# Kernel optimization log

Measured on AMD Instinct MI355X. Metric: run time of the kernel, lower is better.

The kernel has to match this reference:

```python
import jax, jax.numpy as jnp
import numpy as np

EPS = 1e-6
BLK = 64          # VSA coarse block size
H = 12            # num attention heads


def _ln(x, w=None, b=None):
    m = jnp.mean(x, -1, keepdims=True)
    v = jnp.mean((x - m) ** 2, -1, keepdims=True)
    y = (x - m) * jax.lax.rsqrt(v + EPS)
    return y * w + b if w is not None else y


def _rms(x, w):
    return x * jax.lax.rsqrt(jnp.mean(x * x, -1, keepdims=True) + EPS) * w


def _rope(x, cos, sin):
    # non-neox (interleaved) rotary; x: [B,S,H,D], cos/sin: [S,D/2]
    x1, x2 = x[..., 0::2], x[..., 1::2]
    c, s = cos[None, :, None, :], sin[None, :, None, :]
    return jnp.stack([x1 * c - x2 * s, x2 * c + x1 * s], -1).reshape(x.shape)


def _attn(q, k, v):
    scale = 1.0 / np.sqrt(q.shape[-1])
    p = jax.nn.softmax(jnp.einsum('bshd,bthd->bhst', q, k) * scale, -1)
    return jnp.einsum('bhst,bthd->bshd', p, v)


def setup_inputs() -> dict:
    key = jax.random.key(0)
    ks = jax.random.split(key, 24)
    B, S, L2, DIM, FFN = 1, 2048, 512, 1536, 8960
    D = DIM // H
    # rope tables
    pos = jnp.arange(S, dtype=jnp.float32)
    inv = 1.0 / (10000.0 ** (jnp.arange(D // 2, dtype=jnp.float32) / (D // 2)))
    ang = pos[:, None] * inv[None, :]
    w = lambda k, shape, fan: jax.random.normal(k, shape, jnp.float32) / np.sqrt(fan)
    return {
        'hidden_states': jax.random.normal(ks[0], (B, S, DIM), jnp.float32),
        'encoder_hidden_states': jax.random.normal(ks[1], (B, L2, DIM), jnp.float32),
        'temb': jax.random.normal(ks[2], (B, 6, DIM), jnp.float32),
        'rope_cos': jnp.cos(ang), 'rope_sin': jnp.sin(ang),
        'scale_shift_table': w(ks[3], (1, 6, DIM), DIM),
        'Wq': w(ks[4], (DIM, DIM), DIM), 'bq': jnp.zeros((DIM,), jnp.float32),
        'Wk': w(ks[5], (DIM, DIM), DIM), 'bk': jnp.zeros((DIM,), jnp.float32),
        'Wv': w(ks[6], (DIM, DIM), DIM), 'bv': jnp.zeros((DIM,), jnp.float32),
        'Wg': w(ks[7], (DIM, DIM), DIM), 'bg': jnp.zeros((DIM,), jnp.float32),
        'Wo': w(ks[8], (DIM, DIM), DIM), 'bo': jnp.zeros((DIM,), jnp.float32),
        'nq_w': jnp.ones((DIM,), jnp.float32), 'nk_w': jnp.ones((DIM,), jnp.float32),
        'saln_w': jnp.ones((DIM,), jnp.float32), 'saln_b': jnp.zeros((DIM,), jnp.float32),
        'cWq': w(ks[9], (DIM, DIM), DIM), 'cbq': jnp.zeros((DIM,), jnp.float32),
        'cWk': w(ks[10], (DIM, DIM), DIM), 'cbk': jnp.zeros((DIM,), jnp.float32),
        'cWv': w(ks[11], (DIM, DIM), DIM), 'cbv': jnp.zeros((DIM,), jnp.float32),
        'cWo': w(ks[12], (DIM, DIM), DIM), 'cbo': jnp.zeros((DIM,), jnp.float32),
        'cnq_w': jnp.ones((DIM,), jnp.float32), 'cnk_w': jnp.ones((DIM,), jnp.float32),
        'W1': w(ks[13], (DIM, FFN), DIM), 'b1': jnp.zeros((FFN,), jnp.float32),
        'W2': w(ks[14], (FFN, DIM), FFN), 'b2': jnp.zeros((DIM,), jnp.float32),
    }


def reference(hidden_states, encoder_hidden_states, temb, rope_cos, rope_sin,
              scale_shift_table, Wq, bq, Wk, bk, Wv, bv, Wg, bg, Wo, bo,
              nq_w, nk_w, saln_w, saln_b,
              cWq, cbq, cWk, cbk, cWv, cbv, cWo, cbo, cnq_w, cnk_w,
              W1, b1, W2, b2):
    B, S, DIM = hidden_states.shape
    D = DIM // H
    # AdaLN modulation
    e = scale_shift_table + temb  # [B,6,DIM]
    shift, scale, gate, c_shift, c_scale, c_gate = [e[:, i:i + 1] for i in range(6)]
    x = hidden_states
    n = _ln(x) * (1.0 + scale) + shift
    # QKV + gate_compress projections, RMSNorm across heads on q/k
    q = _rms(n @ Wq + bq, nq_w).reshape(B, S, H, D)
    k = _rms(n @ Wk + bk, nk_w).reshape(B, S, H, D)
    v = (n @ Wv + bv).reshape(B, S, H, D)
    g = (n @ Wg + bg).reshape(B, S, H, D)
    q = _rope(q, rope_cos, rope_sin)
    k = _rope(k, rope_cos, rope_sin)
    # VSA: fine (dense, all blocks selected) + gated coarse (block-mean-pooled)
    fine = _attn(q, k, v)
    Nb = S // BLK
    qc = q.reshape(B, Nb, BLK, H, D).mean(2)
    kc = k.reshape(B, Nb, BLK, H, D).mean(2)
    vc = v.reshape(B, Nb, BLK, H, D).mean(2)
    coarse = jnp.repeat(_attn(qc, kc, vc), BLK, axis=1)  # [B,S,H,D]
    ao = (fine + coarse * g).reshape(B, S, DIM) @ Wo + bo
    # self-attn residual + affine LN (null shift/scale)
    hidden = x + gate * ao
    n2 = _ln(hidden, saln_w, saln_b)
    # T2V cross attention
    cq = _rms(n2 @ cWq + cbq, cnq_w).reshape(B, S, H, D)
    ck = _rms(encoder_hidden_states @ cWk + cbk, cnk_w).reshape(B, -1, H, D)
    cv = (encoder_hidden_states @ cWv + cbv).reshape(B, -1, H, D)
    co = _attn(cq, ck, cv).reshape(B, S, DIM) @ cWo + cbo
    hidden = hidden + co
    n3 = _ln(hidden) * (1.0 + c_scale) + c_shift
    # FFN with tanh-approx GELU, gated residual
    ffn = jax.nn.gelu(n3 @ W1 + b1, approximate=True) @ W2 + b2
    return hidden + c_gate * ffn
```

## Files before the change

### kernel.cpp

```cpp
#include <hip/hip_runtime.h>

#define DIMH 1536
#define NH 12
#define DH 128
#define SQ 2048
#define SKV 512
#define FFNH 8960

typedef short short8v __attribute__((ext_vector_type(8)));
typedef short short4v __attribute__((ext_vector_type(4)));
typedef float f32x4 __attribute__((ext_vector_type(4)));

union U8 { unsigned short u[8]; short8v v; };
union U4 { unsigned short u[4]; short4v v; };

__device__ __forceinline__ unsigned short f2bf(float f) {
  unsigned int u = __float_as_uint(f);
  u += 0x7fffu + ((u >> 16) & 1u);
  return (unsigned short)(u >> 16);
}
__device__ __forceinline__ float bf2f(unsigned short u) {
  return __uint_as_float((unsigned int)u << 16);
}

__device__ __forceinline__ void gld16(const void* g, void* l) {
  __builtin_amdgcn_global_load_lds(
      (const __attribute__((address_space(1))) unsigned int*)g,
      (__attribute__((address_space(3))) unsigned int*)l, 16, 0, 0);
}


__global__ void prep_e(const float* __restrict__ sst, const float* __restrict__ temb,
                       float* __restrict__ e) {
  int i = blockIdx.x * 256 + threadIdx.x;
  if (i < 6 * DIMH) e[i] = sst[i] + temb[i];
}

__global__ void concat4(const float* __restrict__ a, const float* __restrict__ b,
                        const float* __restrict__ c, const float* __restrict__ d,
                        float* __restrict__ o) {
  int i = blockIdx.x * 256 + threadIdx.x;
  int which = i / DIMH, r = i - which * DIMH;
  float v;
  if (which == 0) v = a[r];
  else if (which == 1) v = b[r];
  else if (which == 2) v = c[r];
  else v = d[r];
  o[i] = v;
}

__global__ void cast_f32_bf16(const float* __restrict__ x, unsigned short* __restrict__ y,
                              int n) {
  int i = blockIdx.x * 256 + threadIdx.x;
  if (i < n) y[i] = f2bf(x[i]);
}

__global__ __launch_bounds__(256) void transpose_bf16(const float* __restrict__ W,
    unsigned short* __restrict__ Wt, int K, int N) {
  __shared__ float T[32][33];
  int n0 = blockIdx.x * 32, k0 = blockIdx.y * 32;
  int tx = threadIdx.x & 31, ty = threadIdx.x >> 5;
#pragma unroll
  for (int p = 0; p < 4; p++)
    T[ty + p * 8][tx] = W[(long)(k0 + ty + p * 8) * N + n0 + tx];
  __syncthreads();
#pragma unroll
  for (int p = 0; p < 4; p++)
    Wt[(long)(n0 + ty + p * 8) * K + k0 + tx] = f2bf(T[tx][ty + p * 8]);
}

__global__ __launch_bounds__(256) void vtrans(const unsigned short* __restrict__ v, int vs,
    unsigned short* __restrict__ vt, int S) {
  __shared__ unsigned short T[32][33];
  int s0 = blockIdx.x * 32, c0 = blockIdx.y * 32;
  int tx = threadIdx.x & 31, ty = threadIdx.x >> 5;
#pragma unroll
  for (int p = 0; p < 4; p++)
    T[ty + p * 8][tx] = v[(long)(s0 + ty + p * 8) * vs + c0 + tx];
  __syncthreads();
  int head = c0 / DH, dbase = c0 - head * DH;
#pragma unroll
  for (int p = 0; p < 4; p++)
    vt[(long)head * DH * S + (long)(dbase + ty + p * 8) * S + s0 + tx] = T[tx][ty + p * 8];
}

__device__ __forceinline__ float blockReduceSum(float val) {
  __shared__ float sm[4];
#pragma unroll
  for (int off = 32; off > 0; off >>= 1) val += __shfl_xor(val, off, 64);
  if ((threadIdx.x & 63) == 0) sm[threadIdx.x >> 6] = val;
  __syncthreads();
  val = sm[0] + sm[1] + sm[2] + sm[3];
  __syncthreads();
  return val;
}

__global__ __launch_bounds__(256) void layernorm_affine(const float* __restrict__ x,
    unsigned short* __restrict__ out, const float* __restrict__ g,
    const float* __restrict__ b, float add1) {
  long row = blockIdx.x;
  int tid = threadIdx.x;
  const float* xr = x + row * DIMH;
  float v[6];
  float s = 0.f;
#pragma unroll
  for (int i = 0; i < 6; i++) { v[i] = xr[tid + i * 256]; s += v[i]; }
  s = blockReduceSum(s);
  float mean = s * (1.f / DIMH);
  float s2 = 0.f;
#pragma unroll
  for (int i = 0; i < 6; i++) { float d = v[i] - mean; s2 += d * d; }
  s2 = blockReduceSum(s2);
  float inv = rsqrtf(s2 * (1.f / DIMH) + 1e-6f);
  unsigned short* o = out + row * DIMH;
#pragma unroll
  for (int i = 0; i < 6; i++) {
    int c = tid + i * 256;
    o[c] = f2bf((v[i] - mean) * inv * (g[c] + add1) + b[c]);
  }
}

__global__ __launch_bounds__(256) void rms_rope(unsigned short* __restrict__ x, int xs,
    const float* __restrict__ w, const float* __restrict__ cosb,
    const float* __restrict__ sinb, int do_rope, float sc) {
  __shared__ float xr[DIMH];
  long row = blockIdx.x;
  int tid = threadIdx.x;
  unsigned short* xp = x + row * xs;
  float ss = 0.f;
#pragma unroll
  for (int i = 0; i < 6; i++) {
    float t = bf2f(xp[tid + i * 256]);
    xr[tid + i * 256] = t;
    ss += t * t;
  }
  ss = blockReduceSum(ss);
  float inv = rsqrtf(ss * (1.f / DIMH) + 1e-6f) * sc;
#pragma unroll
  for (int j = 0; j < 3; j++) {
    int p = tid + j * 256;
    int h = p >> 6, i = p & 63;
    int d1 = h * DH + 2 * i;
    float v1 = xr[d1] * inv * w[d1];
    float v2 = xr[d1 + 1] * inv * w[d1 + 1];
    float o1 = v1, o2 = v2;
    if (do_rope) {
      float c = cosb[row * 64 + i], s = sinb[row * 64 + i];
      o1 = v1 * c - v2 * s;
      o2 = v2 * c + v1 * s;
    }
    xp[d1] = f2bf(o1);
    xp[d1 + 1] = f2bf(o2);
  }
}

__global__ void pool64(const unsigned short* __restrict__ src, int ss,
                       float* __restrict__ dst) {
  int c = blockIdx.x * 256 + threadIdx.x;
  int nb = blockIdx.y;
  float s = 0.f;
  for (int j = 0; j < 64; j++) s += bf2f(src[(long)(nb * 64 + j) * ss + c]);
  dst[nb * DIMH + c] = s * (1.f / 64.f);
}

__global__ void combine_fine(unsigned short* __restrict__ fine,
                             const float* __restrict__ coarse,
                             const unsigned short* __restrict__ g, int gs) {
  int i = blockIdx.x * 256 + threadIdx.x;
  int srow = i / DIMH, c = i - srow * DIMH;
  fine[i] = f2bf(bf2f(fine[i]) + coarse[(srow >> 6) * DIMH + c] * bf2f(g[(long)srow * gs + c]));
}


__global__ __launch_bounds__(256) void coarse_attn(const float* __restrict__ qc,
    const float* __restrict__ kc, const float* __restrict__ vc, float* __restrict__ co) {
  __shared__ float S[32 * 33];
  int h = blockIdx.x, tid = threadIdx.x;
  for (int e = tid; e < 1024; e += 256) {
    int i = e >> 5, j = e & 31;
    float d = 0.f;
    for (int d0 = 0; d0 < DH; d0++)
      d += qc[i * DIMH + h * DH + d0] * kc[j * DIMH + h * DH + d0];
    S[i * 33 + j] = d;
  }
  __syncthreads();
  if (tid < 32) {
    float m = -3.4e38f;
    for (int j = 0; j < 32; j++) m = fmaxf(m, S[tid * 33 + j]);
    float sum = 0.f;
    for (int j = 0; j < 32; j++) {
      float p = __expf(S[tid * 33 + j] - m);
      S[tid * 33 + j] = p;
      sum += p;
    }
    float r = 1.f / sum;
    for (int j = 0; j < 32; j++) S[tid * 33 + j] *= r;
  }
  __syncthreads();
  for (int e = tid; e < 32 * DH; e += 256) {
    int i = e >> 7, d = e & 127;
    float o = 0.f;
    for (int j = 0; j < 32; j++) o += S[i * 33 + j] * vc[j * DIMH + h * DH + d];
    co[i * DIMH + h * DH + d] = o;
  }
}


#define LDP 68

__global__ __launch_bounds__(128) void flash2(const unsigned short* __restrict__ Q, int qs,
    const unsigned short* __restrict__ Kx, int kstr, const unsigned short* __restrict__ Vt,
    unsigned short* __restrict__ O, int ostr, int Sk) {
  __shared__ unsigned short P[2][16 * LDP];
  int tid = threadIdx.x;
  int w = tid >> 6, lane = tid & 63;
  int quad = lane >> 4, l16 = lane & 15;
  int h = blockIdx.y;
  long q0 = (long)blockIdx.x * 32 + w * 16;
  const unsigned short* Vh = Vt + (long)h * DH * Sk;
  unsigned short* Pw = P[w];

  short8v qf[4];
  {
    const unsigned short* qp = Q + (q0 + l16) * qs + h * DH + quad * 8;
#pragma unroll
    for (int kt = 0; kt < 4; kt++) qf[kt] = *(const short8v*)(qp + kt * 32);
  }
  float m_i = -3.4e38f, l_i = 0.f;
  f32x4 o[8];
#pragma unroll
  for (int nt = 0; nt < 8; nt++) o[nt] = (f32x4){0.f, 0.f, 0.f, 0.f};

  for (int t0 = 0; t0 < Sk; t0 += 64) {
    f32x4 sc[4];
#pragma unroll
    for (int tt = 0; tt < 4; tt++) {
      f32x4 a = (f32x4){0.f, 0.f, 0.f, 0.f};
      const unsigned short* kp = Kx + (long)(t0 + tt * 16 + l16) * kstr + h * DH + quad * 8;
#pragma unroll
      for (int kt = 0; kt < 4; kt++)
        a = __builtin_amdgcn_mfma_f32_16x16x32_bf16(*(const short8v*)(kp + kt * 32),
                                                    qf[kt], a, 0, 0, 0);
      sc[tt] = a;
    }
    float mx = -3.4e38f;
#pragma unroll
    for (int tt = 0; tt < 4; tt++)
#pragma unroll
      for (int r = 0; r < 4; r++) mx = fmaxf(mx, sc[tt][r]);
    mx = fmaxf(mx, __shfl_xor(mx, 16, 64));
    mx = fmaxf(mx, __shfl_xor(mx, 32, 64));
    float mnew = fmaxf(m_i, mx);
    float rs = 0.f;
#pragma unroll
    for (int tt = 0; tt < 4; tt++) {
      U4 pk;
#pragma unroll
      for (int r = 0; r < 4; r++) {
        float pe = __expf(sc[tt][r] - mnew);
        rs += pe;
        pk.u[r] = f2bf(pe);
      }
      *(short4v*)&Pw[l16 * LDP + tt * 16 + quad * 4] = pk.v;
    }
    rs += __shfl_xor(rs, 16, 64);
    rs += __shfl_xor(rs, 32, 64);
    float alpha = __expf(m_i - mnew);
    l_i = l_i * alpha + rs;
    m_i = mnew;
    float ar[4];
#pragma unroll
    for (int r = 0; r < 4; r++) ar[r] = __shfl(alpha, quad * 4 + r, 16);
#pragma unroll
    for (int nt = 0; nt < 8; nt++) {
      f32x4 t = o[nt];
      t[0] *= ar[0]; t[1] *= ar[1]; t[2] *= ar[2]; t[3] *= ar[3];
      o[nt] = t;
    }
#pragma unroll
    for (int c = 0; c < 2; c++) {
      short8v ap = *(const short8v*)&Pw[l16 * LDP + c * 32 + quad * 8];
#pragma unroll
      for (int nt = 0; nt < 8; nt++) {
        short8v bv = *(const short8v*)&Vh[(long)(nt * 16 + l16) * Sk + t0 + c * 32 + quad * 8];
        o[nt] = __builtin_amdgcn_mfma_f32_16x16x32_bf16(ap, bv, o[nt], 0, 0, 0);
      }
    }
  }
  float linv[4];
#pragma unroll
  for (int r = 0; r < 4; r++) linv[r] = 1.f / __shfl(l_i, quad * 4 + r, 16);
#pragma unroll
  for (int nt = 0; nt < 8; nt++)
#pragma unroll
    for (int r = 0; r < 4; r++)
      O[(q0 + quad * 4 + r) * ostr + h * DH + nt * 16 + l16] = f2bf(o[nt][r] * linv[r]);
}


__global__ __launch_bounds__(256) void gemm3(const unsigned short* __restrict__ A, int lda,
    const unsigned short* __restrict__ Wt, const float* __restrict__ bias,
    void* __restrict__ outv, int ldc, const float* __restrict__ res,
    const float* __restrict__ gvec, int M, int N, int K, int kchunk, int mode) {
  __shared__ unsigned short As[128 * 64];
  __shared__ unsigned short Bs[128 * 64];
  int tid = threadIdx.x;
  int m0 = blockIdx.x * 128, n0 = blockIdx.y * 128;
  int wave = tid >> 6, lane = tid & 63;
  int quad = lane >> 4, l16 = lane & 15;
  int wm = (wave & 1) * 64, wn = (wave >> 1) * 64;
  int k0 = blockIdx.z * kchunk;
  int k1 = k0 + kchunk; if (k1 > K) k1 = K;

  int rofs = lane >> 3;
  int schunk = (lane & 7) ^ rofs;
  const unsigned short* Ag = A + (long)(m0 + wave * 32 + rofs) * lda + schunk * 8;
  const unsigned short* Bg = Wt + (long)(n0 + wave * 32 + rofs) * (long)K + schunk * 8;
  unsigned short* Albase = &As[(wave * 32) * 64];
  unsigned short* Blbase = &Bs[(wave * 32) * 64];

  f32x4 acc[4][4];
#pragma unroll
  for (int mt = 0; mt < 4; mt++)
#pragma unroll
    for (int nt = 0; nt < 4; nt++) acc[mt][nt] = (f32x4){0.f, 0.f, 0.f, 0.f};

  for (int kb = k0; kb < k1; kb += 64) {
    __syncthreads();
#pragma unroll
    for (int j = 0; j < 4; j++) {
      gld16(Ag + (long)(j * 8) * lda + kb, Albase + (j * 8) * 64);
      gld16(Bg + (long)(j * 8) * K + kb, Blbase + (j * 8) * 64);
    }
    __syncthreads();
#pragma unroll
    for (int ks = 0; ks < 2; ks++) {
      short8v af[4], bfr[4];
#pragma unroll
      for (int mt = 0; mt < 4; mt++) {
        int r = wm + mt * 16 + l16;
        af[mt] = *(const short8v*)&As[r * 64 + (((ks * 4 + quad) ^ (r & 7)) * 8)];
      }
#pragma unroll
      for (int nt = 0; nt < 4; nt++) {
        int r = wn + nt * 16 + l16;
        bfr[nt] = *(const short8v*)&Bs[r * 64 + (((ks * 4 + quad) ^ (r & 7)) * 8)];
      }
#pragma unroll
      for (int mt = 0; mt < 4; mt++)
#pragma unroll
        for (int nt = 0; nt < 4; nt++)
          acc[mt][nt] = __builtin_amdgcn_mfma_f32_16x16x32_bf16(af[mt], bfr[nt], acc[mt][nt], 0, 0, 0);
    }
  }

  long zoff = (mode == 3) ? (long)blockIdx.z * M * (long)ldc : 0;
#pragma unroll
  for (int mt = 0; mt < 4; mt++)
#pragma unroll
    for (int nt = 0; nt < 4; nt++)
#pragma unroll
      for (int r = 0; r < 4; r++) {
        int row = m0 + wm + mt * 16 + quad * 4 + r;
        int col = n0 + wn + nt * 16 + l16;
        float v = acc[mt][nt][r];
        if (bias) v += bias[col];
        if (mode == 1) {
          float z = 0.7978845608028654f * (v + 0.044715f * v * v * v);
          float e2 = __expf(2.f * z);
          float th_ = 1.f - 2.f / (e2 + 1.f);
          v = 0.5f * v * (1.f + th_);
        }
        long idx = (long)row * ldc + col;
        if (mode == 2) {
          float gv = gvec ? gvec[col] : 1.f;
          ((float*)outv)[idx] = res[idx] + gv * v;
        } else {
          ((unsigned short*)outv)[zoff + idx] = f2bf(v);
        }
      }
}

__global__ void reduce_splitk(const unsigned short* __restrict__ p, int nsplit,
                              const float* __restrict__ hid, const float* __restrict__ b2,
                              const float* __restrict__ gvec, float* __restrict__ out) {
  int i = blockIdx.x * 256 + threadIdx.x;
  int c = i % DIMH;
  float s = 0.f;
  for (int z = 0; z < nsplit; z++) s += bf2f(p[(long)z * SQ * DIMH + i]);
  out[i] = hid[i] + gvec[c] * (s + b2[c]);
}


extern "C" void kernel_launch(void* const* d_in, const int* in_sizes, int n_in,
                              void* d_out, int out_size, void* d_ws, size_t ws_size,
                              hipStream_t stream) {
  (void)in_sizes; (void)n_in; (void)out_size;
  const float* hs   = (const float*)d_in[0];
  const float* enc  = (const float*)d_in[1];
  const float* temb = (const float*)d_in[2];
  const float* rc   = (const float*)d_in[3];
  const float* rsn  = (const float*)d_in[4];
  const float* sst  = (const float*)d_in[5];
  const float* Wq = (const float*)d_in[6];   const float* bq = (const float*)d_in[7];
  const float* Wk = (const float*)d_in[8];   const float* bk = (const float*)d_in[9];
  const float* Wv = (const float*)d_in[10];  const float* bv = (const float*)d_in[11];
  const float* Wg = (const float*)d_in[12];  const float* bg = (const float*)d_in[13];
  const float* Wo = (const float*)d_in[14];  const float* bo = (const float*)d_in[15];
  const float* nq_w = (const float*)d_in[16];  const float* nk_w = (const float*)d_in[17];
  const float* saln_w = (const float*)d_in[18]; const float* saln_b = (const float*)d_in[19];
  const float* cWq = (const float*)d_in[20]; const float* cbq = (const float*)d_in[21];
  const float* cWk = (const float*)d_in[22]; const float* cbk = (const float*)d_in[23];
  const float* cWv = (const float*)d_in[24]; const float* cbv = (const float*)d_in[25];
  const float* cWo = (const float*)d_in[26]; const float* cbo = (const float*)d_in[27];
  const float* cnq_w = (const float*)d_in[28]; const float* cnk_w = (const float*)d_in[29];
  const float* W1 = (const float*)d_in[30];  const float* b1 = (const float*)d_in[31];
  const float* W2 = (const float*)d_in[32];  const float* b2 = (const float*)d_in[33];
  float* outp = (float*)d_out;
  const float attn_scale = 0.08838834764831845f;

  char* base = (char*)d_ws;
  size_t off = 0;
  auto alloc = [&](size_t bytes) -> void* {
    void* p = (void*)(base + off);
    off += (bytes + 255) & ~(size_t)255;
    return p;
  };
  const long ACTE = (long)SQ * DIMH;
  float* e     = (float*)alloc(6 * DIMH * 4);
  float* bias4 = (float*)alloc(4 * DIMH * 4);
  unsigned short* nbuf = (unsigned short*)alloc(ACTE * 2);
  unsigned short* R    = (unsigned short*)alloc((size_t)SQ * FFNH * 2);
  float* hid           = (float*)alloc(ACTE * 4);
  unsigned short* WT   = (unsigned short*)alloc((size_t)FFNH * DIMH * 2);
  unsigned short* vt   = (unsigned short*)alloc((size_t)NH * DH * SQ * 2);
  unsigned short* encb = (unsigned short*)alloc((size_t)SKV * DIMH * 2);
  float* qc  = (float*)alloc(32 * DIMH * 4);
  float* kc  = (float*)alloc(32 * DIMH * 4);
  float* vc  = (float*)alloc(32 * DIMH * 4);
  float* cob = (float*)alloc(32 * DIMH * 4);
  size_t fixed_off = off;
  int nsplit = 4;
  unsigned short* parts = (unsigned short*)alloc((size_t)4 * ACTE * 2);
  if (off > ws_size) { off = fixed_off; nsplit = 2; parts = (unsigned short*)alloc((size_t)2 * ACTE * 2); }
  if (off > ws_size) { nsplit = 1; }

  unsigned short* qkvg = R;
  unsigned short* qb   = R;
  unsigned short* kb   = R + DIMH;
  unsigned short* vb   = R + 2 * DIMH;
  unsigned short* gb   = R + 3 * DIMH;
  unsigned short* fine = R + 4 * ACTE;
  unsigned short* qb2  = R;
  unsigned short* kb2  = R + ACTE;
  unsigned short* vb2  = R + ACTE + (long)SKV * DIMH;
  unsigned short* f1   = R;

  prep_e<<<36, 256, 0, stream>>>(sst, temb, e);
  concat4<<<24, 256, 0, stream>>>(bq, bk, bv, bg, bias4);

  layernorm_affine<<<SQ, 256, 0, stream>>>(hs, nbuf, e + DIMH, e, 1.f);

  dim3 tsq(DIMH / 32, DIMH / 32);
  transpose_bf16<<<tsq, 256, 0, stream>>>(Wq, WT + 0L * DIMH * DIMH, DIMH, DIMH);
  transpose_bf16<<<tsq, 256, 0, stream>>>(Wk, WT + 1L * DIMH * DIMH, DIMH, DIMH);
  transpose_bf16<<<tsq, 256, 0, stream>>>(Wv, WT + 2L * DIMH * DIMH, DIMH, DIMH);
  transpose_bf16<<<tsq, 256, 0, stream>>>(Wg, WT + 3L * DIMH * DIMH, DIMH, DIMH);
  gemm3<<<dim3(SQ / 128, 4 * DIMH / 128), 256, 0, stream>>>(
      nbuf, DIMH, WT, bias4, qkvg, 4 * DIMH, nullptr, nullptr, SQ, 4 * DIMH, DIMH, DIMH, 0);

  rms_rope<<<SQ, 256, 0, stream>>>(qb, 4 * DIMH, nq_w, rc, rsn, 1, attn_scale);
  rms_rope<<<SQ, 256, 0, stream>>>(kb, 4 * DIMH, nk_w, rc, rsn, 1, 1.f);

  pool64<<<dim3(6, 32), 256, 0, stream>>>(qb, 4 * DIMH, qc);
  pool64<<<dim3(6, 32), 256, 0, stream>>>(kb, 4 * DIMH, kc);
  pool64<<<dim3(6, 32), 256, 0, stream>>>(vb, 4 * DIMH, vc);

  vtrans<<<dim3(SQ / 32, DIMH / 32), 256, 0, stream>>>(vb, 4 * DIMH, vt, SQ);
  flash2<<<dim3(SQ / 32, NH), 128, 0, stream>>>(qb, 4 * DIMH, kb, 4 * DIMH, vt,
                                                fine, DIMH, SQ);
  coarse_attn<<<NH, 256, 0, stream>>>(qc, kc, vc, cob);
  combine_fine<<<SQ * DIMH / 256, 256, 0, stream>>>(fine, cob, gb, 4 * DIMH);

  transpose_bf16<<<tsq, 256, 0, stream>>>(Wo, WT, DIMH, DIMH);
  gemm3<<<dim3(SQ / 128, DIMH / 128), 256, 0, stream>>>(
      fine, DIMH, WT, bo, hid, DIMH, hs, e + 2 * DIMH, SQ, DIMH, DIMH, DIMH, 2);

  layernorm_affine<<<SQ, 256, 0, stream>>>(hid, nbuf, saln_w, saln_b, 0.f);
  transpose_bf16<<<tsq, 256, 0, stream>>>(cWq, WT, DIMH, DIMH);
  gemm3<<<dim3(SQ / 128, DIMH / 128), 256, 0, stream>>>(
      nbuf, DIMH, WT, cbq, qb2, DIMH, nullptr, nullptr, SQ, DIMH, DIMH, DIMH, 0);
  rms_rope<<<SQ, 256, 0, stream>>>(qb2, DIMH, cnq_w, nullptr, nullptr, 0, attn_scale);

  cast_f32_bf16<<<SKV * DIMH / 256, 256, 0, stream>>>(enc, encb, SKV * DIMH);
  transpose_bf16<<<tsq, 256, 0, stream>>>(cWk, WT, DIMH, DIMH);
  gemm3<<<dim3(SKV / 128, DIMH / 128), 256, 0, stream>>>(
      encb, DIMH, WT, cbk, kb2, DIMH, nullptr, nullptr, SKV, DIMH, DIMH, DIMH, 0);
  transpose_bf16<<<tsq, 256, 0, stream>>>(cWv, WT, DIMH, DIMH);
  gemm3<<<dim3(SKV / 128, DIMH / 128), 256, 0, stream>>>(
      encb, DIMH, WT, cbv, vb2, DIMH, nullptr, nullptr, SKV, DIMH, DIMH, DIMH, 0);
  rms_rope<<<SKV, 256, 0, stream>>>(kb2, DIMH, cnk_w, nullptr, nullptr, 0, 1.f);

  vtrans<<<dim3(SKV / 32, DIMH / 32), 256, 0, stream>>>(vb2, DIMH, vt, SKV);
  flash2<<<dim3(SQ / 32, NH), 128, 0, stream>>>(qb2, DIMH, kb2, DIMH, vt,
                                                fine, DIMH, SKV);
  transpose_bf16<<<tsq, 256, 0, stream>>>(cWo, WT, DIMH, DIMH);
  gemm3<<<dim3(SQ / 128, DIMH / 128), 256, 0, stream>>>(
      fine, DIMH, WT, cbo, hid, DIMH, hid, nullptr, SQ, DIMH, DIMH, DIMH, 2);

  layernorm_affine<<<SQ, 256, 0, stream>>>(hid, nbuf, e + 4 * DIMH, e + 3 * DIMH, 1.f);
  transpose_bf16<<<dim3(FFNH / 32, DIMH / 32), 256, 0, stream>>>(W1, WT, DIMH, FFNH);
  gemm3<<<dim3(SQ / 128, FFNH / 128), 256, 0, stream>>>(
      nbuf, DIMH, WT, b1, f1, FFNH, nullptr, nullptr, SQ, FFNH, DIMH, DIMH, 1);
  transpose_bf16<<<dim3(DIMH / 32, FFNH / 32), 256, 0, stream>>>(W2, WT, FFNH, DIMH);
  if (nsplit == 1) {
    gemm3<<<dim3(SQ / 128, DIMH / 128), 256, 0, stream>>>(
        f1, FFNH, WT, b2, outp, DIMH, hid, e + 5 * DIMH, SQ, DIMH, FFNH, FFNH, 2);
  } else {
    gemm3<<<dim3(SQ / 128, DIMH / 128, nsplit), 256, 0, stream>>>(
        f1, FFNH, WT, nullptr, parts, DIMH, nullptr, nullptr, SQ, DIMH, FFNH, FFNH / nsplit, 3);
    reduce_splitk<<<SQ * DIMH / 256, 256, 0, stream>>>(parts, nsplit, hid, b2,
                                                       e + 5 * DIMH, outp);
  }
}
```

Measured before the change: 1.186 ms.

## Split flash attention over key chunks and merge partials in combine kernel

Adds a split-KV (flash-decoding style) mode to flash2. Each z-slice processes a chunk of keys and writes unnormalized bf16 partial outputs plus per-row max and sum. A new attn_combine kernel merges these with log-sum-exp weights. The goal is more blocks in flight, since the original grid is only 64x12 blocks of 128 threads and may underfill the GPU. The cost is extra global traffic for the partials, an extra launch, and bf16 rounding of the unnormalized partials.

```diff
diff --git a/kernel.cpp b/kernel.cpp
--- a/kernel.cpp
+++ b/kernel.cpp
@@ -210,16 +210,22 @@
 
 __global__ __launch_bounds__(128) void flash2(const unsigned short* __restrict__ Q, int qs,
     const unsigned short* __restrict__ Kx, int kstr, const unsigned short* __restrict__ Vt,
-    unsigned short* __restrict__ O, int ostr, int Sk) {
+    unsigned short* __restrict__ O, int ostr, int Sk,
+    float* __restrict__ ml, long zstride, int skchunk) {
   __shared__ unsigned short P[2][16 * LDP];
   int tid = threadIdx.x;
   int w = tid >> 6, lane = tid & 63;
   int quad = lane >> 4, l16 = lane & 15;
   int h = blockIdx.y;
+  int bz = blockIdx.z;
   long q0 = (long)blockIdx.x * 32 + w * 16;
   const unsigned short* Vh = Vt + (long)h * DH * Sk;
   unsigned short* Pw = P[w];
 
+  int t_begin = bz * skchunk;
+  int t_end = t_begin + skchunk;
+  if (t_end > Sk) t_end = Sk;
+
   short8v qf[4];
   {
     const unsigned short* qp = Q + (q0 + l16) * qs + h * DH + quad * 8;
@@ -231,7 +237,7 @@
 #pragma unroll
   for (int nt = 0; nt < 8; nt++) o[nt] = (f32x4){0.f, 0.f, 0.f, 0.f};
 
-  for (int t0 = 0; t0 < Sk; t0 += 64) {
+  for (int t0 = t_begin; t0 < t_end; t0 += 64) {
     f32x4 sc[4];
 #pragma unroll
     for (int tt = 0; tt < 4; tt++) {
@@ -287,14 +293,65 @@
       }
     }
   }
-  float linv[4];
-#pragma unroll
-  for (int r = 0; r < 4; r++) linv[r] = 1.f / __shfl(l_i, quad * 4 + r, 16);
-#pragma unroll
-  for (int nt = 0; nt < 8; nt++)
-#pragma unroll
-    for (int r = 0; r < 4; r++)
-      O[(q0 + quad * 4 + r) * ostr + h * DH + nt * 16 + l16] = f2bf(o[nt][r] * linv[r]);
+  if (ml) {
+    if (quad == 0) {
+      float* mlp = ml + ((size_t)(bz * NH + h) * SQ + q0 + l16) * 2;
+      mlp[0] = m_i;
+      mlp[1] = l_i;
+    }
+    unsigned short* Ow = O + (long)bz * zstride;
+#pragma unroll
+    for (int nt = 0; nt < 8; nt++)
+#pragma unroll
+      for (int r = 0; r < 4; r++)
+        Ow[(q0 + quad * 4 + r) * ostr + h * DH + nt * 16 + l16] = f2bf(o[nt][r]);
+  } else {
+    float linv[4];
+#pragma unroll
+    for (int r = 0; r < 4; r++) linv[r] = 1.f / __shfl(l_i, quad * 4 + r, 16);
+#pragma unroll
+    for (int nt = 0; nt < 8; nt++)
+#pragma unroll
+      for (int r = 0; r < 4; r++)
+        O[(q0 + quad * 4 + r) * ostr + h * DH + nt * 16 + l16] = f2bf(o[nt][r] * linv[r]);
+  }
+}
+
+__global__ __launch_bounds__(192) void attn_combine(const unsigned short* __restrict__ parts,
+    const float* __restrict__ ml, int nz, unsigned short* __restrict__ fine, int fstr) {
+  __shared__ float wgt[4][NH];
+  __shared__ float linv[NH];
+  int q = blockIdx.x, tid = threadIdx.x;
+  if (tid < NH) {
+    float m = -3.4e38f;
+    for (int z = 0; z < nz; z++)
+      m = fmaxf(m, ml[((size_t)(z * NH + tid) * SQ + q) * 2]);
+    float l = 0.f;
+    for (int z = 0; z < nz; z++) {
+      const float* p = &ml[((size_t)(z * NH + tid) * SQ + q) * 2];
+      float wz = __expf(p[0] - m);
+      wgt[z][tid] = wz;
+      l += p[1] * wz;
+    }
+    linv[tid] = 1.f / l;
+  }
+  __syncthreads();
+  int c0 = tid * 8, h = c0 >> 7;
+  float acc[8];
+#pragma unroll
+  for (int j = 0; j < 8; j++) acc[j] = 0.f;
+  for (int z = 0; z < nz; z++) {
+    U8 pv;
+    pv.v = *(const short8v*)&parts[(size_t)z * SQ * DIMH + (size_t)q * DIMH + c0];
+    float wz = wgt[z][h];
+#pragma unroll
+    for (int j = 0; j < 8; j++) acc[j] += bf2f(pv.u[j]) * wz;
+  }
+  U8 ov;
+  float li = linv[h];
+#pragma unroll
+  for (int j = 0; j < 8; j++) ov.u[j] = f2bf(acc[j] * li);
+  *(short8v*)&fine[(size_t)q * fstr + c0] = ov.v;
 }
 
 
@@ -439,11 +496,13 @@
   float* kc  = (float*)alloc(32 * DIMH * 4);
   float* vc  = (float*)alloc(32 * DIMH * 4);
   float* cob = (float*)alloc(32 * DIMH * 4);
+  float* mlbuf = (float*)alloc((size_t)4 * NH * SQ * 2 * 4);
   size_t fixed_off = off;
   int nsplit = 4;
   unsigned short* parts = (unsigned short*)alloc((size_t)4 * ACTE * 2);
   if (off > ws_size) { off = fixed_off; nsplit = 2; parts = (unsigned short*)alloc((size_t)2 * ACTE * 2); }
   if (off > ws_size) { nsplit = 1; }
+  int asplit = (nsplit >= 4) ? 4 : ((nsplit == 2) ? 2 : 1);
 
   unsigned short* qkvg = R;
   unsigned short* qb   = R;
@@ -477,9 +536,16 @@
   pool64<<<dim3(6, 32), 256, 0, stream>>>(vb, 4 * DIMH, vc);
 
   vtrans<<<dim3(SQ / 32, DIMH / 32), 256, 0, stream>>>(vb, 4 * DIMH, vt, SQ);
-  flash2<<<dim3(SQ / 32, NH), 128, 0, stream>>>(qb, 4 * DIMH, kb, 4 * DIMH, vt,
-                                                fine, DIMH, SQ);
-  coarse_attn<<<NH, 256, 0, stream>>>(qc, kc, vc, cob);
+  if (asplit > 1) {
+    flash2<<<dim3(SQ / 32, NH, asplit), 128, 0, stream>>>(qb, 4 * DIMH, kb, 4 * DIMH, vt,
+        parts, DIMH, SQ, mlbuf, ACTE, SQ / asplit);
+    coarse_attn<<<NH, 256, 0, stream>>>(qc, kc, vc, cob);
+    attn_combine<<<SQ, 192, 0, stream>>>(parts, mlbuf, asplit, fine, DIMH);
+  } else {
+    flash2<<<dim3(SQ / 32, NH), 128, 0, stream>>>(qb, 4 * DIMH, kb, 4 * DIMH, vt,
+                                                  fine, DIMH, SQ, nullptr, 0, SQ);
+    coarse_attn<<<NH, 256, 0, stream>>>(qc, kc, vc, cob);
+  }
   combine_fine<<<SQ * DIMH / 256, 256, 0, stream>>>(fine, cob, gb, 4 * DIMH);
 
   transpose_bf16<<<tsq, 256, 0, stream>>>(Wo, WT, DIMH, DIMH);
@@ -502,8 +568,14 @@
   rms_rope<<<SKV, 256, 0, stream>>>(kb2, DIMH, cnk_w, nullptr, nullptr, 0, 1.f);
 
   vtrans<<<dim3(SKV / 32, DIMH / 32), 256, 0, stream>>>(vb2, DIMH, vt, SKV);
-  flash2<<<dim3(SQ / 32, NH), 128, 0, stream>>>(qb2, DIMH, kb2, DIMH, vt,
-                                                fine, DIMH, SKV);
+  if (asplit > 1) {
+    flash2<<<dim3(SQ / 32, NH, asplit), 128, 0, stream>>>(qb2, DIMH, kb2, DIMH, vt,
+        parts, DIMH, SKV, mlbuf, ACTE, SKV / asplit);
+    attn_combine<<<SQ, 192, 0, stream>>>(parts, mlbuf, asplit, fine, DIMH);
+  } else {
+    flash2<<<dim3(SQ / 32, NH), 128, 0, stream>>>(qb2, DIMH, kb2, DIMH, vt,
+                                                  fine, DIMH, SKV, nullptr, 0, SKV);
+  }
   transpose_bf16<<<tsq, 256, 0, stream>>>(cWo, WT, DIMH, DIMH);
   gemm3<<<dim3(SQ / 128, DIMH / 128), 256, 0, stream>>>(
       fine, DIMH, WT, cbo, hid, DIMH, hid, nullptr, SQ, DIMH, DIMH, DIMH, 2);
```

Result: slower. 1.211 ms (+2.1%).
